# Performance work log

Hardware: AMD Instinct MI355X
Metric: run time of the kernel (lower is better)

Reference implementation:

```python
import jax, jax.numpy as jnp
import numpy as np

B, S, V, H, NH, DFF, L, T = 16, 256, 30522, 768, 12, 3072, 12, 9
DH = H // NH
LN_EPS = 1e-12


def _ln(x, g, b):
    m = x.mean(-1, keepdims=True)
    v = ((x - m) ** 2).mean(-1, keepdims=True)
    return (x - m) * jax.lax.rsqrt(v + LN_EPS) * g + b


def setup_inputs() -> dict:
    key = jax.random.key(0)
    ks = jax.random.split(key, 20)
    n = lambda k, shp: jax.random.normal(k, shp, jnp.float32) * 0.02
    return {
        "x": jax.random.randint(ks[0], (B, S), 0, V),
        "target": jax.random.randint(ks[1], (B, S), 0, T),
        "word_emb": n(ks[2], (V, H)),
        "pos_emb": n(ks[3], (S, H)),
        "type_emb": n(ks[4], (2, H)),
        "emb_ln_g": jnp.ones((H,)), "emb_ln_b": jnp.zeros((H,)),
        "Wq": n(ks[5], (L, H, H)), "bq": jnp.zeros((L, H)),
        "Wk": n(ks[6], (L, H, H)), "bk": jnp.zeros((L, H)),
        "Wv": n(ks[7], (L, H, H)), "bv": jnp.zeros((L, H)),
        "Wo": n(ks[8], (L, H, H)), "bo": jnp.zeros((L, H)),
        "ln1_g": jnp.ones((L, H)), "ln1_b": jnp.zeros((L, H)),
        "W1": n(ks[9], (L, H, DFF)), "b1": jnp.zeros((L, DFF)),
        "W2": n(ks[10], (L, DFF, H)), "b2": jnp.zeros((L, H)),
        "ln2_g": jnp.ones((L, H)), "ln2_b": jnp.zeros((L, H)),
        "clf_W": n(ks[11], (H, T)), "clf_b": jnp.zeros((T,)),
        "crf_start": jax.random.uniform(ks[12], (T,), jnp.float32, -0.1, 0.1),
        "crf_trans": jax.random.uniform(ks[13], (T, T), jnp.float32, -0.1, 0.1),
        "crf_end": jax.random.uniform(ks[14], (T,), jnp.float32, -0.1, 0.1),
    }


def _forward(x, target, word_emb, pos_emb, type_emb, emb_ln_g, emb_ln_b,
             Wq, bq, Wk, bk, Wv, bv, Wo, bo, ln1_g, ln1_b,
             W1, b1, W2, b2, ln2_g, ln2_b, clf_W, clf_b,
             crf_start, crf_trans, crf_end):
    # ---- BERT-base encoder (post-LN), no attention mask (all tokens valid) ----
    h = _ln(word_emb[x] + pos_emb[None, :, :] + type_emb[0][None, None, :], emb_ln_g, emb_ln_b)
    scale = 1.0 / np.sqrt(DH).astype(np.float32)
    for l in range(L):
        q = (h @ Wq[l] + bq[l]).reshape(B, S, NH, DH)
        k = (h @ Wk[l] + bk[l]).reshape(B, S, NH, DH)
        v = (h @ Wv[l] + bv[l]).reshape(B, S, NH, DH)
        att = jax.nn.softmax(jnp.einsum('bqhd,bkhd->bhqk', q, k) * scale, axis=-1)
        ctx = jnp.einsum('bhqk,bkhd->bqhd', att, v).reshape(B, S, H)
        h = _ln(h + ctx @ Wo[l] + bo[l], ln1_g[l], ln1_b[l])
        ff = jax.nn.gelu(h @ W1[l] + b1[l], approximate=False) @ W2[l] + b2[l]
        h = _ln(h + ff, ln2_g[l], ln2_b[l])

    logits = h @ clf_W + clf_b  # [B,S,T] emissions

    # ---- CRF negative log-likelihood (torchcrf semantics, reduction='mean') ----
    mask = target > -1                      # [B,S] bool
    tags = jnp.where(mask, target, 0)
    bidx = jnp.arange(B)
    emit = jnp.take_along_axis(logits, tags[..., None], axis=-1)[..., 0]  # [B,S]

    # numerator: score of the gold path
    num = crf_start[tags[:, 0]] + emit[:, 0]
    trans = crf_trans[tags[:, :-1], tags[:, 1:]]                          # [B,S-1]
    num = num + jnp.sum((trans + emit[:, 1:]) * mask[:, 1:], axis=1)
    last = jnp.sum(mask.astype(jnp.int32), axis=1) - 1
    num = num + crf_end[tags[bidx, last]]

    # denominator: forward algorithm (logsumexp recurrence over time)
    alpha0 = crf_start[None, :] + logits[:, 0]                            # [B,T]

    def step(alpha, xs):
        em, m = xs                                                        # [B,T], [B]
        nxt = jax.nn.logsumexp(alpha[:, :, None] + crf_trans[None], axis=1) + em
        return jnp.where(m[:, None], nxt, alpha), None

    alpha, _ = jax.lax.scan(step, alpha0,
                            (jnp.swapaxes(logits[:, 1:], 0, 1),
                             jnp.swapaxes(mask[:, 1:], 0, 1)))
    denom = jax.nn.logsumexp(alpha + crf_end[None, :], axis=1)

    llh = num - denom
    return -jnp.mean(llh)  # model returns -loss where loss = mean log-likelihood


def reference(x, target, word_emb, pos_emb, type_emb, emb_ln_g, emb_ln_b,
              Wq, bq, Wk, bk, Wv, bv, Wo, bo, ln1_g, ln1_b,
              W1, b1, W2, b2, ln2_g, ln2_b, clf_W, clf_b,
              crf_start, crf_trans, crf_end):
    return _forward(x, target, word_emb, pos_emb, type_emb, emb_ln_g, emb_ln_b,
                    Wq, bq, Wk, bk, Wv, bv, Wo, bo, ln1_g, ln1_b,
                    W1, b1, W2, b2, ln2_g, ln2_b, clf_W, clf_b,
                    crf_start, crf_trans, crf_end)
```

## Files before the change

kernel.cpp:

```cpp
#include <hip/hip_runtime.h>
#include <math.h>

#define B 16
#define S 256
#define H 768
#define NH 12
#define DH 64
#define DFF 3072
#define L 12
#define T 9
#define M (B*S)
#define LN_EPS 1e-12f
#define QKVS (3*H)
#define NCH 16

typedef __attribute__((ext_vector_type(8))) __bf16 bf16x8;
typedef __attribute__((ext_vector_type(8))) unsigned short u16x8;
typedef __attribute__((ext_vector_type(4))) unsigned short u16x4;
typedef __attribute__((ext_vector_type(4))) float f32x4;

__device__ __forceinline__ unsigned short f2bf(float f) {
    unsigned int u = __float_as_uint(f);
    unsigned int r = u + 0x7fffu + ((u >> 16) & 1u);
    return (unsigned short)(r >> 16);
}
__device__ __forceinline__ float bf2f(unsigned short h) {
    return __uint_as_float((unsigned int)h << 16);
}

__global__ void convT_kernel(const float* __restrict__ W, unsigned short* __restrict__ WT,
                             int K, int N, size_t dstLayerStride) {
    __shared__ float tile[32][33];
    const int layer = blockIdx.z;
    const float* Wp = W + (size_t)layer * K * N;
    unsigned short* Tp = WT + (size_t)layer * dstLayerStride;
    const int n0 = blockIdx.x * 32, k0 = blockIdx.y * 32;
    const int tx = threadIdx.x, ty = threadIdx.y;
#pragma unroll
    for (int i = 0; i < 32; i += 8)
        tile[ty + i][tx] = Wp[(size_t)(k0 + ty + i) * N + n0 + tx];
    __syncthreads();
    {
        const int u = ty * 32 + tx;
        const int r = u >> 3, kq = (u & 7) << 2;
        u16x4 o;
#pragma unroll
        for (int j = 0; j < 4; ++j) o[j] = f2bf(tile[kq + j][r]);
        *(u16x4*)&Tp[(size_t)(n0 + r) * K + k0 + kq] = o;
    }
}

__global__ void biascat_kernel(const float* __restrict__ bq, const float* __restrict__ bk,
                               const float* __restrict__ bv, float* __restrict__ out) {
    int idx = blockIdx.x * 256 + threadIdx.x;
    if (idx >= L * QKVS) return;
    int l = idx / QKVS, c = idx % QKVS;
    float v = (c < H) ? bq[l * H + c] : (c < 2 * H) ? bk[l * H + c - H] : bv[l * H + c - 2 * H];
    out[idx] = v;
}

__global__ void embed_ln_kernel(const int* __restrict__ x,
                                const float* __restrict__ word_emb,
                                const float* __restrict__ pos_emb,
                                const float* __restrict__ type_emb,
                                const float* __restrict__ g,
                                const float* __restrict__ bta,
                                float* __restrict__ h,
                                unsigned short* __restrict__ hb) {
    const int row = blockIdx.x;
    const int s = row % S;
    const int tok = x[row];
    const int t = threadIdx.x;
    const int c = t << 2;
    const float4 wv = *(const float4*)&word_emb[(size_t)tok * H + c];
    const float4 pv = *(const float4*)&pos_emb[s * H + c];
    const float4 tv = *(const float4*)&type_emb[c];
    float v[4] = {wv.x + pv.x + tv.x, wv.y + pv.y + tv.y, wv.z + pv.z + tv.z, wv.w + pv.w + tv.w};
    float s1 = v[0] + v[1] + v[2] + v[3];
    float s2 = v[0]*v[0] + v[1]*v[1] + v[2]*v[2] + v[3]*v[3];
#pragma unroll
    for (int o = 32; o; o >>= 1) { s1 += __shfl_xor(s1, o); s2 += __shfl_xor(s2, o); }
    __shared__ float ws[3][2];
    const int w = t >> 6, l = t & 63;
    if (l == 0) { ws[w][0] = s1; ws[w][1] = s2; }
    __syncthreads();
    const float S1 = ws[0][0] + ws[1][0] + ws[2][0];
    const float S2 = ws[0][1] + ws[1][1] + ws[2][1];
    const float mean = S1 * (1.0f / H);
    const float var = fmaxf(S2 * (1.0f / H) - mean * mean, 0.f);
    const float inv = rsqrtf(var + LN_EPS);
    const float4 gv = *(const float4*)&g[c];
    const float4 bv = *(const float4*)&bta[c];
    float4 outv;
    outv.x = (v[0] - mean) * inv * gv.x + bv.x;
    outv.y = (v[1] - mean) * inv * gv.y + bv.y;
    outv.z = (v[2] - mean) * inv * gv.z + bv.z;
    outv.w = (v[3] - mean) * inv * gv.w + bv.w;
    *(float4*)&h[(size_t)row * H + c] = outv;
    u16x4 ob = {f2bf(outv.x), f2bf(outv.y), f2bf(outv.z), f2bf(outv.w)};
    *(u16x4*)&hb[(size_t)row * H + c] = ob;
}

__global__ void residual_ln_kernel(float* __restrict__ h,
                                   const float* __restrict__ delta,
                                   const float* __restrict__ g,
                                   const float* __restrict__ bta,
                                   unsigned short* __restrict__ hb) {
    const int row = blockIdx.x;
    const int t = threadIdx.x;
    const int c = t << 2;
    const float4 hv = *(const float4*)&h[(size_t)row * H + c];
    const float4 dv = *(const float4*)&delta[(size_t)row * H + c];
    float v[4] = {hv.x + dv.x, hv.y + dv.y, hv.z + dv.z, hv.w + dv.w};
    float s1 = v[0] + v[1] + v[2] + v[3];
    float s2 = v[0]*v[0] + v[1]*v[1] + v[2]*v[2] + v[3]*v[3];
#pragma unroll
    for (int o = 32; o; o >>= 1) { s1 += __shfl_xor(s1, o); s2 += __shfl_xor(s2, o); }
    __shared__ float ws[3][2];
    const int w = t >> 6, l = t & 63;
    if (l == 0) { ws[w][0] = s1; ws[w][1] = s2; }
    __syncthreads();
    const float S1 = ws[0][0] + ws[1][0] + ws[2][0];
    const float S2 = ws[0][1] + ws[1][1] + ws[2][1];
    const float mean = S1 * (1.0f / H);
    const float var = fmaxf(S2 * (1.0f / H) - mean * mean, 0.f);
    const float inv = rsqrtf(var + LN_EPS);
    const float4 gv = *(const float4*)&g[c];
    const float4 bv = *(const float4*)&bta[c];
    float4 outv;
    outv.x = (v[0] - mean) * inv * gv.x + bv.x;
    outv.y = (v[1] - mean) * inv * gv.y + bv.y;
    outv.z = (v[2] - mean) * inv * gv.z + bv.z;
    outv.w = (v[3] - mean) * inv * gv.w + bv.w;
    *(float4*)&h[(size_t)row * H + c] = outv;
    u16x4 ob = {f2bf(outv.x), f2bf(outv.y), f2bf(outv.z), f2bf(outv.w)};
    *(u16x4*)&hb[(size_t)row * H + c] = ob;
}

#define LSTR 72

template<int ACT, int WF, int WB, int MR>
__global__ __launch_bounds__(256, (MR == 2 ? 3 : 2))
void gemm_bf16(const unsigned short* __restrict__ A,
               const unsigned short* __restrict__ WT,
               const float* __restrict__ bias,
               float* __restrict__ Cf,
               unsigned short* __restrict__ Cb,
               int K, int N) {
    __shared__ unsigned short lA[MR * 32 * LSTR];
    __shared__ unsigned short lB[128 * LSTR];
    const int tid = threadIdx.x;
    const int m0 = blockIdx.y * (MR * 32), n0 = blockIdx.x << 7;
    const int l = tid & 63, w = tid >> 6;
    const int wr = w >> 1, wc = w & 1;
    const int lr = l & 15, kg = l >> 4;

    const int srow = tid >> 3, scol = (tid & 7) << 3;
    const unsigned short* gA = A + (size_t)(m0 + srow) * K + scol;
    const unsigned short* gB = WT + (size_t)(n0 + srow) * K + scol;

    f32x4 acc[MR][4];
#pragma unroll
    for (int i = 0; i < MR; ++i)
#pragma unroll
        for (int j = 0; j < 4; ++j) acc[i][j] = (f32x4){0.f, 0.f, 0.f, 0.f};

    u16x8 ra[MR], rb[4];
#pragma unroll
    for (int p = 0; p < MR; ++p) ra[p] = *(const u16x8*)(gA + (size_t)p * 32 * K);
#pragma unroll
    for (int p = 0; p < 4; ++p) rb[p] = *(const u16x8*)(gB + (size_t)p * 32 * K);

    for (int kt = 0; kt < K; kt += 64) {
#pragma unroll
        for (int p = 0; p < MR; ++p)
            *(u16x8*)&lA[(srow + p * 32) * LSTR + scol] = ra[p];
#pragma unroll
        for (int p = 0; p < 4; ++p)
            *(u16x8*)&lB[(srow + p * 32) * LSTR + scol] = rb[p];
        __syncthreads();
        if (kt + 64 < K) {
#pragma unroll
            for (int p = 0; p < MR; ++p) ra[p] = *(const u16x8*)(gA + (size_t)p * 32 * K + kt + 64);
#pragma unroll
            for (int p = 0; p < 4; ++p) rb[p] = *(const u16x8*)(gB + (size_t)p * 32 * K + kt + 64);
        }
#pragma unroll
        for (int ks = 0; ks < 2; ++ks) {
            bf16x8 af[MR], bfr[4];
#pragma unroll
            for (int m = 0; m < MR; ++m)
                af[m] = *(const bf16x8*)&lA[(wr * (MR * 16) + (m << 4) + lr) * LSTR + ks * 32 + (kg << 3)];
#pragma unroll
            for (int n = 0; n < 4; ++n)
                bfr[n] = *(const bf16x8*)&lB[((wc << 6) + (n << 4) + lr) * LSTR + ks * 32 + (kg << 3)];
#pragma unroll
            for (int m = 0; m < MR; ++m)
#pragma unroll
                for (int n = 0; n < 4; ++n)
                    acc[m][n] = __builtin_amdgcn_mfma_f32_16x16x32_bf16(af[m], bfr[n], acc[m][n], 0, 0, 0);
        }
        __syncthreads();
    }

    const int rbase = m0 + wr * (MR * 16) + (kg << 2);
    const int cbase = n0 + (wc << 6) + lr;
#pragma unroll
    for (int m = 0; m < MR; ++m) {
#pragma unroll
        for (int n = 0; n < 4; ++n) {
            const int col = cbase + (n << 4);
            const float bv = bias[col];
#pragma unroll
            for (int j = 0; j < 4; ++j) {
                const int row = rbase + (m << 4) + j;
                float v = acc[m][n][j] + bv;
                if (ACT == 1) v = 0.5f * v * (1.0f + erff(v * 0.70710678118654752440f));
                if (WF) Cf[(size_t)row * N + col] = v;
                if (WB) Cb[(size_t)row * N + col] = f2bf(v);
            }
        }
    }
}

__global__ __launch_bounds__(256, 2)
void attn_mfma(const unsigned short* __restrict__ qkv,
               unsigned short* __restrict__ ctxb) {
    __shared__ unsigned short Ks[256 * 72];
    __shared__ unsigned short Vt[64 * 264];
    __shared__ unsigned short Ps[4][16 * 72];

    const int blk = blockIdx.x;
    const int half = blk & 1;
    const int hh = (blk >> 1) % NH;
    const int b = blk / (2 * NH);
    const int t = threadIdx.x;
    const int l = t & 63, w = t >> 6;
    const int l15 = l & 15, g = l >> 4;

    {
        const int c0 = (t & 7) << 3;
        int r = t >> 3;
#pragma unroll
        for (int it = 0; it < 8; ++it, r += 32) {
            u16x8 kv = *(const u16x8*)&qkv[(size_t)(b * S + r) * QKVS + H + hh * 64 + c0];
            *(u16x8*)&Ks[r * 72 + c0] = kv;
        }
    }
    {
        const int d0 = (t & 7) << 3;
        int s = t >> 3;
#pragma unroll
        for (int it = 0; it < 8; ++it, s += 32) {
            u16x8 vv = *(const u16x8*)&qkv[(size_t)(b * S + s) * QKVS + 2 * H + hh * 64 + d0];
#pragma unroll
            for (int j = 0; j < 8; ++j) {
                int d = d0 + j;
                Vt[d * 264 + (s ^ (((d >> 3) & 7) << 3))] = vv[j];
            }
        }
    }
    __syncthreads();

    unsigned short* ps = Ps[w];
#pragma unroll
    for (int qi = 0; qi < 2; ++qi) {
        const int qrow = half * 128 + qi * 64 + w * 16 + l15;
        const unsigned short* qp = &qkv[(size_t)(b * S + qrow) * QKVS + hh * 64 + g * 8];
        bf16x8 aq0 = *(const bf16x8*)qp;
        bf16x8 aq1 = *(const bf16x8*)(qp + 32);

        f32x4 acc[16];
#pragma unroll
        for (int n = 0; n < 16; ++n) acc[n] = (f32x4){0.f, 0.f, 0.f, 0.f};
        __builtin_amdgcn_s_setprio(1);
#pragma unroll
        for (int n = 0; n < 16; ++n) {
            const unsigned short* kp = &Ks[(n * 16 + l15) * 72 + g * 8];
            bf16x8 b0 = *(const bf16x8*)kp;
            bf16x8 b1 = *(const bf16x8*)(kp + 32);
            acc[n] = __builtin_amdgcn_mfma_f32_16x16x32_bf16(aq0, b0, acc[n], 0, 0, 0);
            acc[n] = __builtin_amdgcn_mfma_f32_16x16x32_bf16(aq1, b1, acc[n], 0, 0, 0);
        }
        __builtin_amdgcn_s_setprio(0);

        float inv[4];
#pragma unroll
        for (int j = 0; j < 4; ++j) {
            float mx = acc[0][j];
#pragma unroll
            for (int n = 1; n < 16; ++n) mx = fmaxf(mx, acc[n][j]);
            mx = fmaxf(mx, __shfl_xor(mx, 1));
            mx = fmaxf(mx, __shfl_xor(mx, 2));
            mx = fmaxf(mx, __shfl_xor(mx, 4));
            mx = fmaxf(mx, __shfl_xor(mx, 8));
            float sum = 0.f;
#pragma unroll
            for (int n = 0; n < 16; ++n) {
                float e = exp2f((acc[n][j] - mx) * 0.18033688011112042f);
                acc[n][j] = e;
                sum += e;
            }
            sum += __shfl_xor(sum, 1);
            sum += __shfl_xor(sum, 2);
            sum += __shfl_xor(sum, 4);
            sum += __shfl_xor(sum, 8);
            inv[j] = 1.0f / sum;
        }

        f32x4 cacc[4];
#pragma unroll
        for (int nd = 0; nd < 4; ++nd) cacc[nd] = (f32x4){0.f, 0.f, 0.f, 0.f};
#pragma unroll
        for (int c = 0; c < 4; ++c) {
#pragma unroll
            for (int nl = 0; nl < 4; ++nl) {
                int n = c * 4 + nl;
#pragma unroll
                for (int j = 0; j < 4; ++j)
                    ps[(g * 4 + j) * 72 + nl * 16 + l15] = f2bf(acc[n][j]);
            }
            bf16x8 pa0 = *(const bf16x8*)&ps[l15 * 72 + g * 8];
            bf16x8 pa1 = *(const bf16x8*)&ps[l15 * 72 + 32 + g * 8];
            __builtin_amdgcn_s_setprio(1);
#pragma unroll
            for (int nd = 0; nd < 4; ++nd) {
                const int d = nd * 16 + l15;
                const int swz = ((d >> 3) & 7) << 3;
                const unsigned short* vp0 = &Vt[d * 264 + ((c * 64 + g * 8) ^ swz)];
                const unsigned short* vp1 = &Vt[d * 264 + ((c * 64 + 32 + g * 8) ^ swz)];
                bf16x8 v0 = *(const bf16x8*)vp0;
                bf16x8 v1 = *(const bf16x8*)vp1;
                cacc[nd] = __builtin_amdgcn_mfma_f32_16x16x32_bf16(pa0, v0, cacc[nd], 0, 0, 0);
                cacc[nd] = __builtin_amdgcn_mfma_f32_16x16x32_bf16(pa1, v1, cacc[nd], 0, 0, 0);
            }
            __builtin_amdgcn_s_setprio(0);
        }

#pragma unroll
        for (int nd = 0; nd < 4; ++nd)
#pragma unroll
            for (int j = 0; j < 4; ++j) {
                int qr = half * 128 + qi * 64 + w * 16 + g * 4 + j;
                ctxb[(size_t)(b * S + qr) * H + hh * 64 + nd * 16 + l15] = f2bf(cacc[nd][j] * inv[j]);
            }
    }
}

__global__ void clf_kernel(const float* __restrict__ h,
                           const float* __restrict__ W,
                           const float* __restrict__ bias,
                           float* __restrict__ logits) {
    const int row = blockIdx.x * 4 + (threadIdx.x >> 6);
    const int l = threadIdx.x & 63;
    const float* hp = h + (size_t)row * H;
    float acc[T] = {};
#pragma unroll
    for (int i = 0; i < 12; ++i) {
        const int k = l + (i << 6);
        const float x = hp[k];
        const float* wp = &W[k * T];
#pragma unroll
        for (int n = 0; n < T; ++n) acc[n] += x * wp[n];
    }
#pragma unroll
    for (int o = 32; o; o >>= 1)
#pragma unroll
        for (int n = 0; n < T; ++n) acc[n] += __shfl_xor(acc[n], o);
    if (l < T) logits[(size_t)row * T + l] = acc[l] + bias[l];
}

__global__ void crf_chunk_kernel(const float* __restrict__ logits,
                                 const int* __restrict__ target,
                                 const float* __restrict__ trans,
                                 float* __restrict__ Tc) {
    const int blk = blockIdx.x;
    const int b = blk >> 4, c = blk & 15;
    const int t = threadIdx.x;
    const int i = t / 9, j = t - i * 9;
    const bool act = t < 81;
    __shared__ float Tb[2][81];
    const float* lg = logits + (size_t)b * S * T;
    const int* tg = target + b * S;
    const float K2 = 1.44269504088896340736f;
    const float IK = 0.69314718055994530942f;

    float trc[T];
    if (act) {
#pragma unroll
        for (int k = 0; k < T; ++k) trc[k] = trans[k * T + j];
        Tb[0][t] = (i == j) ? 0.f : -1e30f;
    }
    __syncthreads();

    int p = 0;
    const int s0 = c * 16 + 1;
    const int s1 = (c == 15) ? S : (s0 + 16);
    for (int s = s0; s < s1; ++s) {
        if (tg[s] > -1) {
            if (act) {
                const float em = lg[s * T + j];
                float v[T];
#pragma unroll
                for (int k = 0; k < T; ++k) v[k] = Tb[p][i * 9 + k] + trc[k];
                float mx = fmaxf(v[0], v[1]);
                mx = fmaxf(mx, fmaxf(v[2], v[3]));
                mx = fmaxf(mx, fmaxf(v[4], v[5]));
                mx = fmaxf(mx, fmaxf(v[6], v[7]));
                mx = fmaxf(mx, v[8]);
                float sum = 0.f;
#pragma unroll
                for (int k = 0; k < T; ++k) sum += exp2f((v[k] - mx) * K2);
                Tb[p ^ 1][t] = mx + IK * log2f(sum) + em;
            }
            __syncthreads();
            p ^= 1;
        }
    }
    if (act) Tc[(size_t)blk * 81 + t] = Tb[p][t];
}

__global__ __launch_bounds__(1024)
void crf_final_kernel(const float* __restrict__ logits,
                      const int* __restrict__ target,
                      const float* __restrict__ start,
                      const float* __restrict__ trans,
                      const float* __restrict__ endv,
                      const float* __restrict__ Tc,
                      float* __restrict__ out) {
    const int t = threadIdx.x;
    const int b = t >> 6, l = t & 63;
    const float* lg = logits + (size_t)b * S * T;
    const int* tg = target + b * S;
    const float K2 = 1.44269504088896340736f;
    const float IK = 0.69314718055994530942f;

    float pnum = 0.f; int pcnt = 0;
#pragma unroll
    for (int c = 0; c < 4; ++c) {
        const int s = 1 + l + (c << 6);
        if (s < S) {
            const int tcur = tg[s], tprev = tg[s - 1];
            const bool m = tcur > -1;
            const int tag = m ? tcur : 0;
            const int ptag = (tprev > -1) ? tprev : 0;
            if (m) { pnum += trans[ptag * T + tag] + lg[s * T + tag]; pcnt += 1; }
        }
    }
#pragma unroll
    for (int o = 32; o; o >>= 1) { pnum += __shfl_xor(pnum, o); pcnt += __shfl_xor(pcnt, o); }

    const int jj = (l < T) ? l : 0;
    float a = start[jj] + lg[jj];
    for (int c = 0; c < NCH; ++c) {
        const float* Tm = Tc + ((size_t)(b * NCH + c)) * 81;
        float v[T];
#pragma unroll
        for (int i2 = 0; i2 < T; ++i2) v[i2] = __shfl(a, i2) + Tm[i2 * 9 + jj];
        float mx = fmaxf(v[0], v[1]);
        mx = fmaxf(mx, fmaxf(v[2], v[3]));
        mx = fmaxf(mx, fmaxf(v[4], v[5]));
        mx = fmaxf(mx, fmaxf(v[6], v[7]));
        mx = fmaxf(mx, v[8]);
        float sum = 0.f;
#pragma unroll
        for (int k = 0; k < T; ++k) sum += exp2f((v[k] - mx) * K2);
        a = mx + IK * log2f(sum);
    }

    float val = (l < T) ? (a + endv[jj]) : -1e30f;
    float mx = val;
#pragma unroll
    for (int o = 8; o; o >>= 1) mx = fmaxf(mx, __shfl_xor(mx, o));
    float sm = (l < T) ? exp2f((val - mx) * K2) : 0.f;
#pragma unroll
    for (int o = 8; o; o >>= 1) sm += __shfl_xor(sm, o);
    const float denom = mx + IK * log2f(sm);

    __shared__ float part[16];
    if (l == 0) {
        const bool m0 = tg[0] > -1;
        const int tag0 = m0 ? tg[0] : 0;
        const int cnt = pcnt + (m0 ? 1 : 0);
        int lastIdx = cnt - 1; if (lastIdx < 0) lastIdx = 0;
        const int lt = tg[lastIdx];
        const int lastTag = (lt > -1) ? lt : 0;
        const float num = start[tag0] + lg[tag0] + pnum + endv[lastTag];
        part[b] = num - denom;
    }
    __syncthreads();
    if (t == 0) {
        float s = 0.f;
#pragma unroll
        for (int i = 0; i < 16; ++i) s += part[i];
        out[0] = -s * (1.0f / 16.0f);
    }
}

extern "C" void kernel_launch(void* const* d_in, const int* in_sizes, int n_in,
                              void* d_out, int out_size, void* d_ws, size_t ws_size,
                              hipStream_t stream) {
    const int*   x        = (const int*)d_in[0];
    const int*   target   = (const int*)d_in[1];
    const float* word_emb = (const float*)d_in[2];
    const float* pos_emb  = (const float*)d_in[3];
    const float* type_emb = (const float*)d_in[4];
    const float* emb_ln_g = (const float*)d_in[5];
    const float* emb_ln_b = (const float*)d_in[6];
    const float* Wq = (const float*)d_in[7];
    const float* bq = (const float*)d_in[8];
    const float* Wk = (const float*)d_in[9];
    const float* bk = (const float*)d_in[10];
    const float* Wv = (const float*)d_in[11];
    const float* bv = (const float*)d_in[12];
    const float* Wo = (const float*)d_in[13];
    const float* bo = (const float*)d_in[14];
    const float* ln1_g = (const float*)d_in[15];
    const float* ln1_b = (const float*)d_in[16];
    const float* W1 = (const float*)d_in[17];
    const float* b1 = (const float*)d_in[18];
    const float* W2 = (const float*)d_in[19];
    const float* b2 = (const float*)d_in[20];
    const float* ln2_g = (const float*)d_in[21];
    const float* ln2_b = (const float*)d_in[22];
    const float* clf_W = (const float*)d_in[23];
    const float* clf_b = (const float*)d_in[24];
    const float* crf_start = (const float*)d_in[25];
    const float* crf_trans = (const float*)d_in[26];
    const float* crf_end   = (const float*)d_in[27];

    char* ws = (char*)d_ws;
    size_t off = 0;
    auto alloc = [&](size_t bytes) { void* p = ws + off; off += (bytes + 255) & ~255ull; return p; };

    unsigned short* wqkvT = (unsigned short*)alloc((size_t)L * 3 * H * H * 2);
    unsigned short* woT   = (unsigned short*)alloc((size_t)L * H * H * 2);
    unsigned short* w1T   = (unsigned short*)alloc((size_t)L * H * DFF * 2);
    unsigned short* w2T   = (unsigned short*)alloc((size_t)L * H * DFF * 2);
    float*          bcat  = (float*)alloc((size_t)L * QKVS * 4);
    float*          h     = (float*)alloc((size_t)M * H * 4);
    unsigned short* hb    = (unsigned short*)alloc((size_t)M * H * 2);
    unsigned short* qkvb  = (unsigned short*)alloc((size_t)M * QKVS * 2);
    unsigned short* ctxb  = (unsigned short*)alloc((size_t)M * H * 2);
    float*          go    = (float*)alloc((size_t)M * H * 4);
    unsigned short* ffb   = (unsigned short*)alloc((size_t)M * DFF * 2);
    float*          logits = (float*)alloc((size_t)M * T * 4);
    float*          Tcbuf  = (float*)alloc((size_t)B * NCH * 81 * 4);

    dim3 tb(32, 8);
    convT_kernel<<<dim3(H / 32, H / 32, L), tb, 0, stream>>>(Wq, wqkvT,             H, H, (size_t)3 * H * H);
    convT_kernel<<<dim3(H / 32, H / 32, L), tb, 0, stream>>>(Wk, wqkvT + H * H,     H, H, (size_t)3 * H * H);
    convT_kernel<<<dim3(H / 32, H / 32, L), tb, 0, stream>>>(Wv, wqkvT + 2 * H * H, H, H, (size_t)3 * H * H);
    convT_kernel<<<dim3(H / 32, H / 32, L), tb, 0, stream>>>(Wo, woT, H, H, (size_t)H * H);
    convT_kernel<<<dim3(DFF / 32, H / 32, L), tb, 0, stream>>>(W1, w1T, H, DFF, (size_t)H * DFF);
    convT_kernel<<<dim3(H / 32, DFF / 32, L), tb, 0, stream>>>(W2, w2T, DFF, H, (size_t)H * DFF);
    biascat_kernel<<<(L * QKVS + 255) / 256, 256, 0, stream>>>(bq, bk, bv, bcat);

    embed_ln_kernel<<<M, 192, 0, stream>>>(x, word_emb, pos_emb, type_emb, emb_ln_g, emb_ln_b, h, hb);

    const dim3 gQKV(QKVS / 128, M / 128);
    const dim3 gH64(H / 128, M / 64);
    const dim3 gFF(DFF / 128, M / 128);

    for (int l = 0; l < L; ++l) {
        gemm_bf16<0, 0, 1, 4><<<gQKV, 256, 0, stream>>>(hb, wqkvT + (size_t)l * 3 * H * H, bcat + l * QKVS,
                                                        nullptr, qkvb, H, QKVS);
        attn_mfma<<<B * NH * 2, 256, 0, stream>>>(qkvb, ctxb);
        gemm_bf16<0, 1, 0, 2><<<gH64, 256, 0, stream>>>(ctxb, woT + (size_t)l * H * H, bo + l * H, go, nullptr, H, H);
        residual_ln_kernel<<<M, 192, 0, stream>>>(h, go, ln1_g + l * H, ln1_b + l * H, hb);
        gemm_bf16<1, 0, 1, 4><<<gFF, 256, 0, stream>>>(hb, w1T + (size_t)l * H * DFF, b1 + l * DFF, nullptr, ffb, H, DFF);
        gemm_bf16<0, 1, 0, 2><<<gH64, 256, 0, stream>>>(ffb, w2T + (size_t)l * H * DFF, b2 + l * H, go, nullptr, DFF, H);
        residual_ln_kernel<<<M, 192, 0, stream>>>(h, go, ln2_g + l * H, ln2_b + l * H, hb);
    }

    clf_kernel<<<M / 4, 256, 0, stream>>>(h, clf_W, clf_b, logits);
    crf_chunk_kernel<<<B * NCH, 128, 0, stream>>>(logits, target, crf_trans, Tcbuf);
    crf_final_kernel<<<1, 1024, 0, stream>>>(logits, target, crf_start, crf_trans, crf_end, Tcbuf, (float*)d_out);
}
```

Measured before the change: 1.964 ms.

## Add 128x256-tile GEMM for QKV/FFN1 and store output-projection deltas in bf16

Adds a gemm_big kernel with a 128x256 output tile, where each wave computes a 64x128 sub-tile with 32 MFMA accumulators, and uses it for the QKV and FFN-up projections. The larger tile raises operand reuse from LDS and halves the number of blocks. Separately, the Wo and W2 GEMMs now write their outputs as bf16 rather than fp32, and the residual LayerNorm reads bf16 deltas, which cuts memory traffic. The costs are fewer blocks (fewer waves to fill the CUs), higher register pressure, and a small precision loss from rounding the residual deltas to bf16.

```diff
diff --git a/kernel.cpp b/kernel.cpp
--- a/kernel.cpp
+++ b/kernel.cpp
@@ -102,7 +102,7 @@
 }
 
 __global__ void residual_ln_kernel(float* __restrict__ h,
-                                   const float* __restrict__ delta,
+                                   const unsigned short* __restrict__ delta,
                                    const float* __restrict__ g,
                                    const float* __restrict__ bta,
                                    unsigned short* __restrict__ hb) {
@@ -110,8 +110,8 @@
     const int t = threadIdx.x;
     const int c = t << 2;
     const float4 hv = *(const float4*)&h[(size_t)row * H + c];
-    const float4 dv = *(const float4*)&delta[(size_t)row * H + c];
-    float v[4] = {hv.x + dv.x, hv.y + dv.y, hv.z + dv.z, hv.w + dv.w};
+    const u16x4 dv4 = *(const u16x4*)&delta[(size_t)row * H + c];
+    float v[4] = {hv.x + bf2f(dv4[0]), hv.y + bf2f(dv4[1]), hv.z + bf2f(dv4[2]), hv.w + bf2f(dv4[3])};
     float s1 = v[0] + v[1] + v[2] + v[3];
     float s2 = v[0]*v[0] + v[1]*v[1] + v[2]*v[2] + v[3]*v[3];
 #pragma unroll
@@ -218,6 +218,88 @@
                 if (ACT == 1) v = 0.5f * v * (1.0f + erff(v * 0.70710678118654752440f));
                 if (WF) Cf[(size_t)row * N + col] = v;
                 if (WB) Cb[(size_t)row * N + col] = f2bf(v);
+            }
+        }
+    }
+}
+
+template<int ACT>
+__global__ __launch_bounds__(256, 2)
+void gemm_big(const unsigned short* __restrict__ A,
+              const unsigned short* __restrict__ WT,
+              const float* __restrict__ bias,
+              unsigned short* __restrict__ Cb,
+              int K, int N) {
+    __shared__ unsigned short lA[128 * LSTR];
+    __shared__ unsigned short lB[256 * LSTR];
+    const int tid = threadIdx.x;
+    const int m0 = blockIdx.y << 7, n0 = blockIdx.x << 8;
+    const int l = tid & 63, w = tid >> 6;
+    const int wr = w >> 1, wc = w & 1;
+    const int lr = l & 15, kg = l >> 4;
+
+    const int srow = tid >> 3, scol = (tid & 7) << 3;
+    const unsigned short* gA = A + (size_t)(m0 + srow) * K + scol;
+    const unsigned short* gB = WT + (size_t)(n0 + srow) * K + scol;
+
+    f32x4 acc[4][8];
+#pragma unroll
+    for (int i = 0; i < 4; ++i)
+#pragma unroll
+        for (int j = 0; j < 8; ++j) acc[i][j] = (f32x4){0.f, 0.f, 0.f, 0.f};
+
+    u16x8 ra[4], rb[8];
+#pragma unroll
+    for (int p = 0; p < 4; ++p) ra[p] = *(const u16x8*)(gA + (size_t)p * 32 * K);
+#pragma unroll
+    for (int p = 0; p < 8; ++p) rb[p] = *(const u16x8*)(gB + (size_t)p * 32 * K);
+
+    for (int kt = 0; kt < K; kt += 64) {
+#pragma unroll
+        for (int p = 0; p < 4; ++p)
+            *(u16x8*)&lA[(srow + p * 32) * LSTR + scol] = ra[p];
+#pragma unroll
+        for (int p = 0; p < 8; ++p)
+            *(u16x8*)&lB[(srow + p * 32) * LSTR + scol] = rb[p];
+        __syncthreads();
+        if (kt + 64 < K) {
+#pragma unroll
+            for (int p = 0; p < 4; ++p) ra[p] = *(const u16x8*)(gA + (size_t)p * 32 * K + kt + 64);
+#pragma unroll
+            for (int p = 0; p < 8; ++p) rb[p] = *(const u16x8*)(gB + (size_t)p * 32 * K + kt + 64);
+        }
+#pragma unroll
+        for (int ks = 0; ks < 2; ++ks) {
+            bf16x8 af[4], bfr[8];
+#pragma unroll
+            for (int m = 0; m < 4; ++m)
+                af[m] = *(const bf16x8*)&lA[((wr << 6) + (m << 4) + lr) * LSTR + ks * 32 + (kg << 3)];
+#pragma unroll
+            for (int n = 0; n < 8; ++n)
+                bfr[n] = *(const bf16x8*)&lB[((wc << 7) + (n << 4) + lr) * LSTR + ks * 32 + (kg << 3)];
+#pragma unroll
+            for (int m = 0; m < 4; ++m)
+#pragma unroll
+                for (int n = 0; n < 8; ++n)
+                    acc[m][n] = __builtin_amdgcn_mfma_f32_16x16x32_bf16(af[m], bfr[n], acc[m][n], 0, 0, 0);
+        }
+        __syncthreads();
+    }
+
+    const int rbase = m0 + (wr << 6) + (kg << 2);
+    const int cbase = n0 + (wc << 7) + lr;
+#pragma unroll
+    for (int m = 0; m < 4; ++m) {
+#pragma unroll
+        for (int n = 0; n < 8; ++n) {
+            const int col = cbase + (n << 4);
+            const float bv = bias[col];
+#pragma unroll
+            for (int j = 0; j < 4; ++j) {
+                const int row = rbase + (m << 4) + j;
+                float v = acc[m][n][j] + bv;
+                if (ACT == 1) v = 0.5f * v * (1.0f + erff(v * 0.70710678118654752440f));
+                Cb[(size_t)row * N + col] = f2bf(v);
             }
         }
     }
@@ -542,7 +624,7 @@
     unsigned short* hb    = (unsigned short*)alloc((size_t)M * H * 2);
     unsigned short* qkvb  = (unsigned short*)alloc((size_t)M * QKVS * 2);
     unsigned short* ctxb  = (unsigned short*)alloc((size_t)M * H * 2);
-    float*          go    = (float*)alloc((size_t)M * H * 4);
+    unsigned short* gob   = (unsigned short*)alloc((size_t)M * H * 2);
     unsigned short* ffb   = (unsigned short*)alloc((size_t)M * DFF * 2);
     float*          logits = (float*)alloc((size_t)M * T * 4);
     float*          Tcbuf  = (float*)alloc((size_t)B * NCH * 81 * 4);
@@ -558,19 +640,18 @@
 
     embed_ln_kernel<<<M, 192, 0, stream>>>(x, word_emb, pos_emb, type_emb, emb_ln_g, emb_ln_b, h, hb);
 
-    const dim3 gQKV(QKVS / 128, M / 128);
+    const dim3 gQKV(QKVS / 256, M / 128);
+    const dim3 gFF1(DFF / 256, M / 128);
     const dim3 gH64(H / 128, M / 64);
-    const dim3 gFF(DFF / 128, M / 128);
 
     for (int l = 0; l < L; ++l) {
-        gemm_bf16<0, 0, 1, 4><<<gQKV, 256, 0, stream>>>(hb, wqkvT + (size_t)l * 3 * H * H, bcat + l * QKVS,
-                                                        nullptr, qkvb, H, QKVS);
+        gemm_big<0><<<gQKV, 256, 0, stream>>>(hb, wqkvT + (size_t)l * 3 * H * H, bcat + l * QKVS, qkvb, H, QKVS);
         attn_mfma<<<B * NH * 2, 256, 0, stream>>>(qkvb, ctxb);
-        gemm_bf16<0, 1, 0, 2><<<gH64, 256, 0, stream>>>(ctxb, woT + (size_t)l * H * H, bo + l * H, go, nullptr, H, H);
-        residual_ln_kernel<<<M, 192, 0, stream>>>(h, go, ln1_g + l * H, ln1_b + l * H, hb);
-        gemm_bf16<1, 0, 1, 4><<<gFF, 256, 0, stream>>>(hb, w1T + (size_t)l * H * DFF, b1 + l * DFF, nullptr, ffb, H, DFF);
-        gemm_bf16<0, 1, 0, 2><<<gH64, 256, 0, stream>>>(ffb, w2T + (size_t)l * H * DFF, b2 + l * H, go, nullptr, DFF, H);
-        residual_ln_kernel<<<M, 192, 0, stream>>>(h, go, ln2_g + l * H, ln2_b + l * H, hb);
+        gemm_bf16<0, 0, 1, 2><<<gH64, 256, 0, stream>>>(ctxb, woT + (size_t)l * H * H, bo + l * H, nullptr, gob, H, H);
+        residual_ln_kernel<<<M, 192, 0, stream>>>(h, gob, ln1_g + l * H, ln1_b + l * H, hb);
+        gemm_big<1><<<gFF1, 256, 0, stream>>>(hb, w1T + (size_t)l * H * DFF, b1 + l * DFF, ffb, H, DFF);
+        gemm_bf16<0, 0, 1, 2><<<gH64, 256, 0, stream>>>(ffb, w2T + (size_t)l * H * DFF, b2 + l * H, nullptr, gob, DFF, H);
+        residual_ln_kernel<<<M, 192, 0, stream>>>(h, gob, ln2_g + l * H, ln2_b + l * H, hb);
     }
 
     clf_kernel<<<M / 4, 256, 0, stream>>>(h, clf_W, clf_b, logits);
```

Result: slower. 2.166 ms (+10.2%).
